# Kernel optimization log

Measured on AMD Instinct MI355X. Metric: run time of the kernel, lower is better.

## Reference

```python
import jax, jax.numpy as jnp
import numpy as np

B, N, D, F = 4096, 64, 64, 4096
KP_DIM = N * (N + 1) // 2  # 2080
# static row-major triu/tril index lists (matches torch.masked_select ordering)
_TRIU_I, _TRIU_J = (np.array(a) for a in np.triu_indices(N, 0))
_TRIL_I, _TRIL_J = (np.array(a) for a in np.tril_indices(N, 0))


def setup_inputs() -> dict:
    key = jax.random.key(0)
    k1, k2, k3, k4 = jax.random.split(key, 4)
    feature_emb = jax.random.normal(k1, (B, N, D), dtype=jnp.float32)
    # xavier_normal for [D, D]
    std = float(np.sqrt(2.0 / (D + D)))
    kp_W = jax.random.normal(k2, (D, D), dtype=jnp.float32) * std
    # nn.Linear weights are [out_features, in_features]
    bound = float(1.0 / np.sqrt(KP_DIM))
    W_triu = jax.random.uniform(k3, (F, KP_DIM), dtype=jnp.float32, minval=-bound, maxval=bound)
    W_tril = jax.random.uniform(k4, (F, KP_DIM), dtype=jnp.float32, minval=-bound, maxval=bound)
    return {"feature_emb": feature_emb, "kp_W": kp_W, "W_triu": W_triu, "W_tril": W_tril}


def reference(feature_emb, kp_W, W_triu, W_tril):
    # embs_kp[b,i,j] = e[b,i,:] @ kp_W @ e[b,j,:]  -> [B, N, N]
    embs_kp = jnp.einsum("bnd,de,bme->bnm", feature_emb, kp_W, feature_emb)
    triu = embs_kp[:, _TRIU_I, _TRIU_J]  # [B, kp_dim], row-major order
    tril = embs_kp[:, _TRIL_I, _TRIL_J]  # [B, kp_dim]
    embs_flatten = feature_emb.reshape(feature_emb.shape[0], -1)  # [B, N*D]
    view_1 = triu @ W_triu.T  # [B, F]
    view_2 = tril @ W_tril.T  # [B, F]
    return (embs_flatten, view_1, view_2)
```

## Files before the change

kernel.cpp:

```cpp
#include <hip/hip_runtime.h>

typedef __bf16 bf16x8 __attribute__((ext_vector_type(8)));
typedef float f32x4 __attribute__((ext_vector_type(4)));
typedef unsigned short u16x4 __attribute__((ext_vector_type(4)));
typedef unsigned short u16x8 __attribute__((ext_vector_type(8)));

__device__ __forceinline__ unsigned short f2bf(float f) {
  unsigned int u = __builtin_bit_cast(unsigned int, f);
  u += 0x7FFFu + ((u >> 16) & 1u);
  return (unsigned short)(u >> 16);
}

__device__ __forceinline__ bf16x8 ld_frag(const unsigned short* p) {
  return __builtin_bit_cast(bf16x8, *(const u16x8*)p);
}

#define MFMA16(a, b, c) __builtin_amdgcn_mfma_f32_16x16x32_bf16((a), (b), (c), 0, 0, 0)

__device__ __forceinline__ void cp16(const void* g, void* l) {
  __builtin_amdgcn_global_load_lds(
      (const __attribute__((address_space(1))) unsigned int*)g,
      (__attribute__((address_space(3))) unsigned int*)l, 16, 0, 0);
}

__global__ __launch_bounds__(256) void cvt_bf16(const float* __restrict__ in,
                                                unsigned short* __restrict__ out,
                                                int n4) {
  int i = blockIdx.x * 256 + threadIdx.x;
  const int stride = gridDim.x * 256;
  for (; i < n4; i += stride) {
    float4 v = ((const float4*)in)[i];
    u16x4 o;
    o[0] = f2bf(v.x); o[1] = f2bf(v.y); o[2] = f2bf(v.z); o[3] = f2bf(v.w);
    ((u16x4*)out)[i] = o;
  }
}

__global__ __launch_bounds__(256) void batch_kp(
    const float* __restrict__ E,
    const float* __restrict__ Wkp,
    float* __restrict__ out0,
    unsigned short* __restrict__ triu,
    unsigned short* __restrict__ tril)
{
  __shared__ __align__(16) unsigned short sE[64 * 64];
  __shared__ __align__(16) unsigned short sWt[64 * 64];
  __shared__ __align__(16) unsigned short sT[64 * 64];

  const int b = blockIdx.x;
  const int tid = threadIdx.x;
  const float* Eb = E + (size_t)b * 4096;
  float* o0 = out0 + (size_t)b * 4096;

#pragma unroll
  for (int it = 0; it < 4; ++it) {
    const int flat = it * 1024 + tid * 4;
    float4 v = *(const float4*)(Eb + flat);
    *(float4*)(o0 + flat) = v;
    u16x4 e;
    e[0] = f2bf(v.x); e[1] = f2bf(v.y); e[2] = f2bf(v.z); e[3] = f2bf(v.w);
    *(u16x4*)(sE + flat) = e;
    float4 wv = *(const float4*)(Wkp + flat);
    const int d = flat >> 6, c0 = flat & 63;
    sWt[(c0 + 0) * 64 + d] = f2bf(wv.x);
    sWt[(c0 + 1) * 64 + d] = f2bf(wv.y);
    sWt[(c0 + 2) * 64 + d] = f2bf(wv.z);
    sWt[(c0 + 3) * 64 + d] = f2bf(wv.w);
  }
  __syncthreads();

  const int lane = tid & 63, w = tid >> 6;
  const int fr = lane & 15;
  const int fk = (lane >> 4) << 3;
  const int qr = (lane >> 4) << 2;

#pragma unroll
  for (int ct = 0; ct < 4; ++ct) {
    f32x4 acc = {0.f, 0.f, 0.f, 0.f};
#pragma unroll
    for (int k2 = 0; k2 < 2; ++k2) {
      bf16x8 a = ld_frag(sE + (w * 16 + fr) * 64 + k2 * 32 + fk);
      bf16x8 bb = ld_frag(sWt + (ct * 16 + fr) * 64 + k2 * 32 + fk);
      acc = MFMA16(a, bb, acc);
    }
#pragma unroll
    for (int r = 0; r < 4; ++r)
      sT[(w * 16 + qr + r) * 64 + ct * 16 + fr] = f2bf(acc[r]);
  }
  __syncthreads();

  unsigned short* tu = triu + (size_t)b * 2080;
  unsigned short* tl = tril + (size_t)b * 2080;
#pragma unroll
  for (int ct = 0; ct < 4; ++ct) {
    f32x4 acc = {0.f, 0.f, 0.f, 0.f};
#pragma unroll
    for (int k2 = 0; k2 < 2; ++k2) {
      bf16x8 a = ld_frag(sT + (w * 16 + fr) * 64 + k2 * 32 + fk);
      bf16x8 bb = ld_frag(sE + (ct * 16 + fr) * 64 + k2 * 32 + fk);
      acc = MFMA16(a, bb, acc);
    }
#pragma unroll
    for (int r = 0; r < 4; ++r) {
      const int i = w * 16 + qr + r;
      const int j = ct * 16 + fr;
      const unsigned short v = f2bf(acc[r]);
      if (j >= i) tu[i * 64 - ((i * (i - 1)) >> 1) + (j - i)] = v;
      if (j <= i) tl[((i * (i + 1)) >> 1) + j] = v;
    }
  }
}

__global__ __launch_bounds__(256) void gemm_views(
    const unsigned short* __restrict__ triu, const unsigned short* __restrict__ tril,
    const unsigned short* __restrict__ Wu, const unsigned short* __restrict__ Wl,
    float* __restrict__ dout)
{
  constexpr int Kd = 2080;
  __shared__ __align__(16) unsigned short sA[128 * 32];
  __shared__ __align__(16) unsigned short sB[128 * 32];

  const int z = blockIdx.z;
  const unsigned short* A = z ? tril : triu;
  const unsigned short* Bw = z ? Wl : Wu;
  float* C = dout + (size_t)16777216 * (size_t)(1 + z);

  const int tid = threadIdx.x;
  const int m0 = blockIdx.y << 7, n0 = blockIdx.x << 7;

  const int tr = tid >> 2, tc = (tid & 3) << 3;
  const unsigned short* ga0 = A + (size_t)(m0 + tr) * Kd + tc;
  const unsigned short* ga1 = ga0 + (size_t)64 * Kd;
  const unsigned short* gb0 = Bw + (size_t)(n0 + tr) * Kd + tc;
  const unsigned short* gb1 = gb0 + (size_t)64 * Kd;
  unsigned short* la0 = sA + tid * 8;
  unsigned short* la1 = sA + 2048 + tid * 8;
  unsigned short* lb0 = sB + tid * 8;
  unsigned short* lb1 = sB + 2048 + tid * 8;

  const int lane = tid & 63, w = tid >> 6;
  const int wm = (w >> 1) << 6, wn = (w & 1) << 6;
  const int fr = lane & 15, fk = (lane >> 4) << 3;

  f32x4 acc[4][4] = {};

  for (int kt = 0; kt < 65; ++kt) {
    const int ko = kt * 32;
    cp16(ga0 + ko, la0);
    cp16(ga1 + ko, la1);
    cp16(gb0 + ko, lb0);
    cp16(gb1 + ko, lb1);
    __syncthreads();

    bf16x8 af[4], bfr[4];
#pragma unroll
    for (int mt = 0; mt < 4; ++mt)
      af[mt] = ld_frag(sA + (wm + mt * 16 + fr) * 32 + fk);
#pragma unroll
    for (int nt = 0; nt < 4; ++nt)
      bfr[nt] = ld_frag(sB + (wn + nt * 16 + fr) * 32 + fk);
#pragma unroll
    for (int mt = 0; mt < 4; ++mt)
#pragma unroll
      for (int nt = 0; nt < 4; ++nt)
        acc[mt][nt] = MFMA16(af[mt], bfr[nt], acc[mt][nt]);
    __syncthreads();
  }

  const int qr = (lane >> 4) << 2;
#pragma unroll
  for (int mt = 0; mt < 4; ++mt) {
#pragma unroll
    for (int nt = 0; nt < 4; ++nt) {
      const int row = m0 + wm + mt * 16 + qr;
      const int col = n0 + wn + nt * 16 + fr;
      float* cp = C + (size_t)row * 4096 + col;
#pragma unroll
      for (int r = 0; r < 4; ++r)
        cp[(size_t)r * 4096] = acc[mt][nt][r];
    }
  }
}

extern "C" void kernel_launch(void* const* d_in, const int* in_sizes, int n_in,
                              void* d_out, int out_size, void* d_ws, size_t ws_size,
                              hipStream_t stream) {
  const float* feat  = (const float*)d_in[0];
  const float* kpW   = (const float*)d_in[1];
  const float* Wtriu = (const float*)d_in[2];
  const float* Wtril = (const float*)d_in[3];
  float* out = (float*)d_out;

  unsigned short* triu_bf = (unsigned short*)d_ws;
  unsigned short* tril_bf = triu_bf + 8519680;
  unsigned short* Wu_bf   = tril_bf + 8519680;
  unsigned short* Wl_bf   = Wu_bf + 8519680;

  cvt_bf16<<<dim3(1024), dim3(256), 0, stream>>>(Wtriu, Wu_bf, 2129920);
  cvt_bf16<<<dim3(1024), dim3(256), 0, stream>>>(Wtril, Wl_bf, 2129920);
  batch_kp<<<dim3(4096), dim3(256), 0, stream>>>(feat, kpW, out, triu_bf, tril_bf);
  gemm_views<<<dim3(32, 32, 2), dim3(256), 0, stream>>>(triu_bf, tril_bf, Wu_bf, Wl_bf, out);
}
```

Measured before the change: 480.0 us.

## Rewrite view GEMM with 256x256 tiles, double-buffered swizzled LDS pipeline

The view GEMM now uses 512-thread blocks computing 256x256 tiles with K=64 steps. It double-buffers global-to-LDS copies with an XOR swizzle and interleaves the loads with MFMA phases using explicit vmcnt waits and setprio. To make the K dimension a whole number of 64-wide steps, the activations and weights are padded from 2080 to 2112 with zeros. The kp_W transpose and bf16 conversion move into a single tiny pre-kernel so each batch block just copies it into LDS. The aim is more reuse per tile, fewer barriers per FLOP and latency hiding, at the cost of more LDS and registers per block and the extra padding traffic.

```diff
diff --git a/kernel.cpp b/kernel.cpp
--- a/kernel.cpp
+++ b/kernel.cpp
@@ -5,6 +5,9 @@
 typedef unsigned short u16x4 __attribute__((ext_vector_type(4)));
 typedef unsigned short u16x8 __attribute__((ext_vector_type(8)));
 
+#define KP 2112
+#define NT 33
+
 __device__ __forceinline__ unsigned short f2bf(float f) {
   unsigned int u = __builtin_bit_cast(unsigned int, f);
   u += 0x7FFFu + ((u >> 16) & 1u);
@@ -23,22 +26,45 @@
       (__attribute__((address_space(3))) unsigned int*)l, 16, 0, 0);
 }
 
-__global__ __launch_bounds__(256) void cvt_bf16(const float* __restrict__ in,
-                                                unsigned short* __restrict__ out,
-                                                int n4) {
+__device__ __forceinline__ void barrier_sync() {
+  asm volatile("" ::: "memory");
+  __builtin_amdgcn_s_barrier();
+  __builtin_amdgcn_sched_barrier(0);
+}
+
+#define VMWAIT(N) asm volatile("s_waitcnt vmcnt(" #N ")" ::: "memory")
+
+__global__ __launch_bounds__(256) void cvt_pad(const float* __restrict__ in,
+                                               unsigned short* __restrict__ out) {
+  const int total = 4096 * (KP / 4);
   int i = blockIdx.x * 256 + threadIdx.x;
   const int stride = gridDim.x * 256;
-  for (; i < n4; i += stride) {
-    float4 v = ((const float4*)in)[i];
-    u16x4 o;
-    o[0] = f2bf(v.x); o[1] = f2bf(v.y); o[2] = f2bf(v.z); o[3] = f2bf(v.w);
+  for (; i < total; i += stride) {
+    const int row = i / (KP / 4);
+    const int c4 = i - row * (KP / 4);
+    u16x4 o = {0, 0, 0, 0};
+    if (c4 < 520) {
+      float4 v = *(const float4*)(in + (size_t)row * 2080 + c4 * 4);
+      o[0] = f2bf(v.x); o[1] = f2bf(v.y); o[2] = f2bf(v.z); o[3] = f2bf(v.w);
+    }
     ((u16x4*)out)[i] = o;
+  }
+}
+
+__global__ __launch_bounds__(256) void prep_wt(const float* __restrict__ W,
+                                               unsigned short* __restrict__ Wt) {
+  const int tid = threadIdx.x;
+#pragma unroll
+  for (int j = 0; j < 16; ++j) {
+    const int o = tid * 16 + j;
+    const int c = o >> 6, d = o & 63;
+    Wt[o] = f2bf(W[d * 64 + c]);
   }
 }
 
 __global__ __launch_bounds__(256) void batch_kp(
     const float* __restrict__ E,
-    const float* __restrict__ Wkp,
+    const unsigned short* __restrict__ Wt,
     float* __restrict__ out0,
     unsigned short* __restrict__ triu,
     unsigned short* __restrict__ tril)
@@ -52,6 +78,9 @@
   const float* Eb = E + (size_t)b * 4096;
   float* o0 = out0 + (size_t)b * 4096;
 
+  cp16(Wt + tid * 8, sWt + tid * 8);
+  cp16(Wt + 2048 + tid * 8, sWt + 2048 + tid * 8);
+
 #pragma unroll
   for (int it = 0; it < 4; ++it) {
     const int flat = it * 1024 + tid * 4;
@@ -60,12 +89,6 @@
     u16x4 e;
     e[0] = f2bf(v.x); e[1] = f2bf(v.y); e[2] = f2bf(v.z); e[3] = f2bf(v.w);
     *(u16x4*)(sE + flat) = e;
-    float4 wv = *(const float4*)(Wkp + flat);
-    const int d = flat >> 6, c0 = flat & 63;
-    sWt[(c0 + 0) * 64 + d] = f2bf(wv.x);
-    sWt[(c0 + 1) * 64 + d] = f2bf(wv.y);
-    sWt[(c0 + 2) * 64 + d] = f2bf(wv.z);
-    sWt[(c0 + 3) * 64 + d] = f2bf(wv.w);
   }
   __syncthreads();
 
@@ -89,8 +112,9 @@
   }
   __syncthreads();
 
-  unsigned short* tu = triu + (size_t)b * 2080;
-  unsigned short* tl = tril + (size_t)b * 2080;
+  unsigned short* tu = triu + (size_t)b * KP;
+  unsigned short* tl = tril + (size_t)b * KP;
+  if (tid < 32) { tu[2080 + tid] = 0; tl[2080 + tid] = 0; }
 #pragma unroll
   for (int ct = 0; ct < 4; ++ct) {
     f32x4 acc = {0.f, 0.f, 0.f, 0.f};
@@ -111,75 +135,111 @@
   }
 }
 
-__global__ __launch_bounds__(256) void gemm_views(
+__global__ __launch_bounds__(512, 2) void gemm_views(
     const unsigned short* __restrict__ triu, const unsigned short* __restrict__ tril,
     const unsigned short* __restrict__ Wu, const unsigned short* __restrict__ Wl,
     float* __restrict__ dout)
 {
-  constexpr int Kd = 2080;
-  __shared__ __align__(16) unsigned short sA[128 * 32];
-  __shared__ __align__(16) unsigned short sB[128 * 32];
+  __shared__ __align__(16) unsigned short lds[65536];
 
   const int z = blockIdx.z;
-  const unsigned short* A = z ? tril : triu;
-  const unsigned short* Bw = z ? Wl : Wu;
+  const unsigned short* Ag = z ? tril : triu;
+  const unsigned short* Bg = z ? Wl : Wu;
   float* C = dout + (size_t)16777216 * (size_t)(1 + z);
 
   const int tid = threadIdx.x;
-  const int m0 = blockIdx.y << 7, n0 = blockIdx.x << 7;
-
-  const int tr = tid >> 2, tc = (tid & 3) << 3;
-  const unsigned short* ga0 = A + (size_t)(m0 + tr) * Kd + tc;
-  const unsigned short* ga1 = ga0 + (size_t)64 * Kd;
-  const unsigned short* gb0 = Bw + (size_t)(n0 + tr) * Kd + tc;
-  const unsigned short* gb1 = gb0 + (size_t)64 * Kd;
-  unsigned short* la0 = sA + tid * 8;
-  unsigned short* la1 = sA + 2048 + tid * 8;
-  unsigned short* lb0 = sB + tid * 8;
-  unsigned short* lb1 = sB + 2048 + tid * 8;
-
-  const int lane = tid & 63, w = tid >> 6;
-  const int wm = (w >> 1) << 6, wn = (w & 1) << 6;
-  const int fr = lane & 15, fk = (lane >> 4) << 3;
-
-  f32x4 acc[4][4] = {};
-
-  for (int kt = 0; kt < 65; ++kt) {
-    const int ko = kt * 32;
-    cp16(ga0 + ko, la0);
-    cp16(ga1 + ko, la1);
-    cp16(gb0 + ko, lb0);
-    cp16(gb1 + ko, lb1);
-    __syncthreads();
-
-    bf16x8 af[4], bfr[4];
-#pragma unroll
-    for (int mt = 0; mt < 4; ++mt)
-      af[mt] = ld_frag(sA + (wm + mt * 16 + fr) * 32 + fk);
-#pragma unroll
-    for (int nt = 0; nt < 4; ++nt)
-      bfr[nt] = ld_frag(sB + (wn + nt * 16 + fr) * 32 + fk);
-#pragma unroll
-    for (int mt = 0; mt < 4; ++mt)
-#pragma unroll
-      for (int nt = 0; nt < 4; ++nt)
-        acc[mt][nt] = MFMA16(af[mt], bfr[nt], acc[mt][nt]);
-    __syncthreads();
-  }
-
-  const int qr = (lane >> 4) << 2;
-#pragma unroll
-  for (int mt = 0; mt < 4; ++mt) {
+  const int lane = tid & 63, wv = tid >> 6;
+  const int m0 = blockIdx.y << 8, n0 = blockIdx.x << 8;
+
+  const int lr = lane >> 3;
+  const int cuch = (lane & 7) ^ lr;
+  const int rA = wv * 8 + lr;
+  const int rB = (wv & 3) * 8 + (wv >> 2) * 64 + lr;
+  const unsigned short* gA = Ag + (size_t)(m0 + rA) * KP + cuch * 8;
+  const unsigned short* gB = Bg + (size_t)(n0 + rB) * KP + cuch * 8;
+  const int dA = tid * 8;
+  const int dB = (wv & 3) * 512 + (wv >> 2) * 4096 + lane * 8;
+
+  const int fr = lane & 15, fq = lane >> 4;
+  const int sx0 = ((fq ^ (fr & 7))) * 8;
+  const int sx1 = (((4 + fq) ^ (fr & 7))) * 8;
+  const int rowA0 = (wv >> 2) * 128 + fr;
+  const int rowB0 = (wv & 3) * 64 + fr;
+
+  f32x4 acc[8][4] = {};
+  bf16x8 af0[4], af1[4], bh0[2], bh1[2];
+
+#define STAGE_A(B_, KT, OFF) do { \
+    cp16(gA + (size_t)(OFF) * KP + (KT) * 64, lds + (B_) * 32768 + (OFF) * 64 + dA); \
+    cp16(gA + (size_t)((OFF) + 128) * KP + (KT) * 64, \
+         lds + (B_) * 32768 + ((OFF) + 128) * 64 + dA); \
+  } while (0)
+#define STAGE_B(B_, KT, OFF) do { \
+    cp16(gB + (size_t)(OFF) * KP + (KT) * 64, \
+         lds + (B_) * 32768 + 16384 + (OFF) * 64 + dB); \
+    cp16(gB + (size_t)((OFF) + 128) * KP + (KT) * 64, \
+         lds + (B_) * 32768 + 16384 + ((OFF) + 128) * 64 + dB); \
+  } while (0)
+
+#define PHASE(B_, MH, NH, LA, LB, STAGE_STMT, WAIT_STMT) do { \
+    if (LA) { \
+      const unsigned short* pa = lds + (B_) * 32768 + ((rowA0 + (MH) * 64) << 6); \
+      _Pragma("unroll") for (int mt = 0; mt < 4; ++mt) { \
+        af0[mt] = ld_frag(pa + mt * 1024 + sx0); \
+        af1[mt] = ld_frag(pa + mt * 1024 + sx1); } } \
+    if (LB) { \
+      const unsigned short* pb = lds + (B_) * 32768 + 16384 + ((rowB0 + (NH) * 32) << 6); \
+      _Pragma("unroll") for (int nt = 0; nt < 2; ++nt) { \
+        bh0[nt] = ld_frag(pb + nt * 1024 + sx0); \
+        bh1[nt] = ld_frag(pb + nt * 1024 + sx1); } } \
+    STAGE_STMT; \
+    barrier_sync(); \
+    __builtin_amdgcn_s_setprio(1); \
+    _Pragma("unroll") for (int mt = 0; mt < 4; ++mt) \
+    _Pragma("unroll") for (int nt = 0; nt < 2; ++nt) { \
+      acc[(MH)*4+mt][(NH)*2+nt] = MFMA16(af0[mt], bh0[nt], acc[(MH)*4+mt][(NH)*2+nt]); \
+      acc[(MH)*4+mt][(NH)*2+nt] = MFMA16(af1[mt], bh1[nt], acc[(MH)*4+mt][(NH)*2+nt]); } \
+    __builtin_amdgcn_s_setprio(0); \
+    WAIT_STMT; \
+    barrier_sync(); \
+  } while (0)
+
+  STAGE_A(0, 0, 0);
+  STAGE_B(0, 0, 0);
+  STAGE_A(0, 0, 64);
+  STAGE_B(0, 0, 32);
+  VMWAIT(4);
+  barrier_sync();
+
+  for (int t = 0; t < NT - 1; ++t) {
+    const int cb = t & 1, nb = cb ^ 1, nk = t + 1;
+    PHASE(cb, 0, 0, 1, 1, STAGE_A(nb, nk, 0),  VMWAIT(4));
+    PHASE(cb, 1, 0, 1, 0, STAGE_B(nb, nk, 0),  VMWAIT(4));
+    PHASE(cb, 1, 1, 0, 1, STAGE_A(nb, nk, 64), (void)0);
+    PHASE(cb, 0, 1, 1, 0, STAGE_B(nb, nk, 32), VMWAIT(4));
+  }
+  {
+    const int cb = (NT - 1) & 1;
+    PHASE(cb, 0, 0, 1, 1, (void)0, VMWAIT(2));
+    PHASE(cb, 1, 0, 1, 0, (void)0, VMWAIT(0));
+    PHASE(cb, 1, 1, 0, 1, (void)0, (void)0);
+    PHASE(cb, 0, 1, 1, 0, (void)0, (void)0);
+  }
+
+  const int qr = fq << 2;
+  const int crow = m0 + (wv >> 2) * 128 + qr;
+  const int ccol = n0 + (wv & 3) * 64 + fr;
+#pragma unroll
+  for (int mt = 0; mt < 8; ++mt)
 #pragma unroll
     for (int nt = 0; nt < 4; ++nt) {
-      const int row = m0 + wm + mt * 16 + qr;
-      const int col = n0 + wn + nt * 16 + fr;
-      float* cp = C + (size_t)row * 4096 + col;
-#pragma unroll
-      for (int r = 0; r < 4; ++r)
-        cp[(size_t)r * 4096] = acc[mt][nt][r];
-    }
-  }
+      float* cp = C + (size_t)(crow + mt * 16) * 4096 + (ccol + nt * 16);
+#pragma unroll
+      for (int r = 0; r < 4; ++r) cp[(size_t)r * 4096] = acc[mt][nt][r];
+    }
+#undef STAGE_A
+#undef STAGE_B
+#undef PHASE
 }
 
 extern "C" void kernel_launch(void* const* d_in, const int* in_sizes, int n_in,
@@ -191,13 +251,16 @@
   const float* Wtril = (const float*)d_in[3];
   float* out = (float*)d_out;
 
+  const size_t per = (size_t)4096 * KP;
   unsigned short* triu_bf = (unsigned short*)d_ws;
-  unsigned short* tril_bf = triu_bf + 8519680;
-  unsigned short* Wu_bf   = tril_bf + 8519680;
-  unsigned short* Wl_bf   = Wu_bf + 8519680;
-
-  cvt_bf16<<<dim3(1024), dim3(256), 0, stream>>>(Wtriu, Wu_bf, 2129920);
-  cvt_bf16<<<dim3(1024), dim3(256), 0, stream>>>(Wtril, Wl_bf, 2129920);
-  batch_kp<<<dim3(4096), dim3(256), 0, stream>>>(feat, kpW, out, triu_bf, tril_bf);
-  gemm_views<<<dim3(32, 32, 2), dim3(256), 0, stream>>>(triu_bf, tril_bf, Wu_bf, Wl_bf, out);
-}
+  unsigned short* tril_bf = triu_bf + per;
+  unsigned short* Wu_bf   = tril_bf + per;
+  unsigned short* Wl_bf   = Wu_bf + per;
+  unsigned short* Wt_bf   = Wl_bf + per;
+
+  cvt_pad<<<dim3(1024), dim3(256), 0, stream>>>(Wtriu, Wu_bf);
+  cvt_pad<<<dim3(1024), dim3(256), 0, stream>>>(Wtril, Wl_bf);
+  prep_wt<<<dim3(1), dim3(256), 0, stream>>>(kpW, Wt_bf);
+  batch_kp<<<dim3(4096), dim3(256), 0, stream>>>(feat, Wt_bf, out, triu_bf, tril_bf);
+  gemm_views<<<dim3(16, 16, 2), dim3(512), 0, stream>>>(triu_bf, tril_bf, Wu_bf, Wl_bf, out);
+}
```

Measured after the change: 429.1 us. -10.6%, faster.
